# Kernel optimization log

Hardware: AMD Instinct MI355X
Metric: run time of the kernel (lower is better)

The kernel has to match this reference:

```python
import jax, jax.numpy as jnp
import numpy as np

B, SIZE, TRACK = 4096, 1024, 1024  # batch, input size, tracker_size


def setup_inputs() -> dict:
    key = jax.random.key(0)
    ks = jax.random.split(key, 9)
    s = 0.02  # small init scale to keep gates in a sane range
    return {
        "top_buf_h": jax.random.normal(ks[0], (B, SIZE), jnp.float32),
        "top_stack1_h": jax.random.normal(ks[1], (B, SIZE), jnp.float32),
        "top_stack2_h": jax.random.normal(ks[2], (B, SIZE), jnp.float32),
        "h_prev": jax.random.normal(ks[3], (B, TRACK), jnp.float32),
        "c_prev": jax.random.normal(ks[4], (B, TRACK), jnp.float32),
        "W_buf": jax.random.normal(ks[5], (SIZE, 4 * TRACK), jnp.float32) * s,
        "W_stack1": jax.random.normal(ks[6], (SIZE, 4 * TRACK), jnp.float32) * s,
        "W_stack2": jax.random.normal(ks[7], (SIZE, 4 * TRACK), jnp.float32) * s,
        "W_lateral": jax.random.normal(ks[8], (TRACK, 4 * TRACK), jnp.float32) * s,
        "b_lateral": jnp.zeros((4 * TRACK,), jnp.float32),
    }


def reference(top_buf_h, top_stack1_h, top_stack2_h, h_prev, c_prev,
              W_buf, W_stack1, W_stack2, W_lateral, b_lateral):
    # Fused tracker step: 3 bias-free projections + lateral projection (with bias)
    gates = (top_buf_h @ W_buf
             + top_stack1_h @ W_stack1
             + top_stack2_h @ W_stack2
             + h_prev @ W_lateral
             + b_lateral)                      # [B, 4*TRACK]
    # SPINN lstm(c_prev, gates): chunk order (a, i, f, o)
    a, i, f, o = jnp.split(gates, 4, axis=1)
    c = jnp.tanh(a) * jax.nn.sigmoid(i) + jax.nn.sigmoid(f) * c_prev
    h = jax.nn.sigmoid(o) * jnp.tanh(c)
    return (h, c)
```

## Files before the change

### kernel.cpp

```cpp
#include <hip/hip_runtime.h>


typedef __bf16 bf16x8 __attribute__((ext_vector_type(8)));
typedef float  f32x4  __attribute__((ext_vector_type(4)));

__device__ __forceinline__ unsigned short f2bf(float x) {
    unsigned int u = __builtin_bit_cast(unsigned int, x);
    u = (u + 0x7fffu + ((u >> 16) & 1u)) >> 16;
    return (unsigned short)u;
}

__device__ __forceinline__ void gl2lds16(const unsigned short* g, unsigned short* l) {
    __builtin_amdgcn_global_load_lds(
        (const __attribute__((address_space(1))) unsigned int*)g,
        (__attribute__((address_space(3))) unsigned int*)l,
        16, 0, 0);
}

__device__ __forceinline__ float sigf(float x) {
    return __builtin_amdgcn_rcpf(1.f + __expf(-x));
}
__device__ __forceinline__ float tanh_fast(float x) {
    return 2.f * __builtin_amdgcn_rcpf(1.f + __expf(-2.f * x)) - 1.f;
}


__global__ void convert_AB(const float* __restrict__ A0, const float* __restrict__ A1,
                           const float* __restrict__ A2, const float* __restrict__ A3,
                           const float* __restrict__ Wb, const float* __restrict__ W1,
                           const float* __restrict__ W2, const float* __restrict__ Wl,
                           unsigned short* __restrict__ Abf,
                           unsigned short* __restrict__ Bt) {
    __shared__ float t[32][33];
    if (blockIdx.x < 16384) {
        int idx = blockIdx.x * 256 + threadIdx.x;
        int e0  = idx * 4;
        int b   = e0 >> 12;
        int k   = e0 & 4095;
        const float* S = (k < 1024) ? A0 : (k < 2048) ? A1 : (k < 3072) ? A2 : A3;
        int col = k & 1023;
        const float4 v = *reinterpret_cast<const float4*>(S + (size_t)b * 1024 + col);
        ushort4 o;
        o.x = f2bf(v.x); o.y = f2bf(v.y); o.z = f2bf(v.z); o.w = f2bf(v.w);
        *reinterpret_cast<ushort4*>(Abf + (size_t)b * 4096 + k) = o;
    } else {
        int tile = blockIdx.x - 16384;
        int jt = tile & 127, kt = tile >> 7;
        int j0 = jt * 32, k0 = kt * 32;
        int ksel = k0 >> 10;
        const float* S = (ksel == 0) ? Wb : (ksel == 1) ? W1 : (ksel == 2) ? W2 : Wl;
        int kloc = k0 & 1023;
        int tx = threadIdx.x & 31, ty = threadIdx.x >> 5;
#pragma unroll
        for (int i = 0; i < 4; ++i) {
            int r = ty + i * 8;
            t[r][tx] = S[(size_t)(kloc + r) * 4096 + j0 + tx];
        }
        __syncthreads();
        int g = j0 >> 10;
        int nbase = j0 & 1023;
#pragma unroll
        for (int i = 0; i < 4; ++i) {
            int jj = ty + i * 8;
            int u  = nbase + jj;
            int p  = (u >> 6) * 256 + ((u >> 4) & 3) * 64 + g * 16 + (u & 15);
            Bt[(size_t)p * 4096 + k0 + tx] = f2bf(t[tx][jj]);
        }
    }
}


__global__ __launch_bounds__(512, 2) void gemm_lstm(
        const unsigned short* __restrict__ A,
        const unsigned short* __restrict__ Bt,
        const float* __restrict__ bias,
        const float* __restrict__ cprev,
        float* __restrict__ out) {
    __shared__ unsigned short lds[65536];
#define ASB(b) (lds + (b) * 16384)
#define BSB(b) (lds + 32768 + (b) * 16384)

    const int tid  = threadIdx.x;
    const int wid  = tid >> 6;
    const int lane = tid & 63;
    const int wm = wid >> 2, wn = wid & 3;
    const int lr = lane & 15, lq = lane >> 4;
    const int bm = blockIdx.y, bc = blockIdx.x;

    const int X0 = wid * 1024 + lane * 16;
    const int rs = X0 >> 7;
    const int cs = ((X0 & 127) ^ ((rs & 7) << 4)) >> 1;
    const unsigned short* Agb = A  + ((size_t)(bm * 256 + rs)) * 4096 + cs;
    const unsigned short* Bgb = Bt + ((size_t)(bc * 256 + rs)) * 4096 + cs;

    const int swz = (lr & 7) << 4;
    const int ca0 = ((lq * 16) ^ swz) >> 1;
    const int ca1 = ((64 + lq * 16) ^ swz) >> 1;

    f32x4 acc[8][4] = {};

#define STAGE_A(b, h, kt) do {                                               \
        unsigned short* _d = ASB(b) + (h) * 8192 + wid * 512;                \
        const unsigned short* _s = Agb + (size_t)((h) * 128) * 4096 + (kt) * 64; \
        gl2lds16(_s, _d);                                                    \
        gl2lds16(_s + 64 * 4096, _d + 4096);                                 \
    } while (0)
#define STAGE_B(b, h, kt) do {                                               \
        unsigned short* _d = BSB(b) + (h) * 8192 + wid * 512;                \
        const unsigned short* _s = Bgb + (size_t)((h) * 128) * 4096 + (kt) * 64; \
        gl2lds16(_s, _d);                                                    \
        gl2lds16(_s + 64 * 4096, _d + 4096);                                 \
    } while (0)
#define LDA(buf, mi, cax) (*reinterpret_cast<const bf16x8*>((buf) + (wm * 128 + (mi) * 16 + lr) * 64 + (cax)))
#define LDB(buf, ni, cax) (*reinterpret_cast<const bf16x8*>((buf) + (wn * 64  + (ni) * 16 + lr) * 64 + (cax)))
#define RD_A(DST, BUF, MI0) do {                                             \
        _Pragma("unroll")                                                    \
        for (int m = 0; m < 2; ++m) {                                        \
            DST[m][0] = LDA(BUF, (MI0) + m, ca0);                            \
            DST[m][1] = LDA(BUF, (MI0) + m, ca1);                            \
        } } while (0)
#define RD_B(DST, BUF) do {                                                  \
        _Pragma("unroll")                                                    \
        for (int n = 0; n < 4; ++n) {                                        \
            DST[n][0] = LDB(BUF, n, ca0);                                    \
            DST[n][1] = LDB(BUF, n, ca1);                                    \
        } } while (0)
#define SBAR() __builtin_amdgcn_s_barrier()
#define VMFENCE() asm volatile("s_waitcnt vmcnt(4)" ::: "memory")
#define MFMA16(P, AF, BF)                                                    \
        __builtin_amdgcn_s_setprio(1);                                       \
        _Pragma("unroll")                                                    \
        for (int m = 0; m < 2; ++m)                                          \
        _Pragma("unroll")                                                    \
        for (int ks = 0; ks < 2; ++ks)                                       \
        _Pragma("unroll")                                                    \
        for (int ni = 0; ni < 4; ++ni)                                       \
            acc[(P)*2 + m][ni] = __builtin_amdgcn_mfma_f32_16x16x32_bf16(    \
                AF[m][ks], BF[ni][ks], acc[(P)*2 + m][ni], 0, 0, 0);         \
        __builtin_amdgcn_s_setprio(0)

#define KITER(T, PAR) do {                                                   \
        const unsigned short* Ac = ASB(PAR);                                 \
        const unsigned short* Bc = BSB(PAR);                                 \
        const int ktA = ((T) < 63) ? (T) + 1 : 63;                           \
        const int ktB = ((T) < 62) ? (T) + 2 : 63;                           \
        STAGE_A(PAR ^ 1, 0, ktA);                                            \
        STAGE_A(PAR ^ 1, 1, ktA);                                            \
        bf16x8 bfr[4][2];                                                    \
        bf16x8 af[2][2];                                                     \
        RD_B(bfr, Bc);                                                       \
        RD_A(af, Ac, 0);                                                     \
        MFMA16(0, af, bfr);                                                  \
        SBAR();     \
        STAGE_B(PAR, 0, ktB);                                                \
        STAGE_B(PAR, 1, ktB);                                                \
        RD_A(af, Ac, 2);                                                     \
        MFMA16(1, af, bfr);                                                  \
        RD_A(af, Ac, 4);                                                     \
        MFMA16(2, af, bfr);                                                  \
        RD_A(af, Ac, 6);                                                     \
        MFMA16(3, af, bfr);                                                  \
        VMFENCE();                                                           \
        SBAR();                          \
    } while (0)

    STAGE_A(0, 0, 0); STAGE_A(0, 1, 0);
    STAGE_B(0, 0, 0); STAGE_B(0, 1, 0);
    STAGE_B(1, 0, 1); STAGE_B(1, 1, 1);
    VMFENCE();
    SBAR();

    for (int u = 0; u < 32; ++u) {
        KITER(2 * u, 0);
        KITER(2 * u + 1, 1);
    }

    const int un = bc * 64 + wn * 16 + lr;
    const float ba  = bias[un];
    const float bi  = bias[1024 + un];
    const float bfv = bias[2048 + un];
    const float bo  = bias[3072 + un];
    float* outh = out;
    float* outc = out + (size_t)4096 * 1024;

#pragma unroll
    for (int mi = 0; mi < 8; ++mi) {
        const int r0 = bm * 256 + wm * 128 + mi * 16 + lq * 4;
#pragma unroll
        for (int r = 0; r < 4; ++r) {
            const size_t off = (size_t)(r0 + r) * 1024 + un;
            const float a  = acc[mi][0][r] + ba;
            const float ii = acc[mi][1][r] + bi;
            const float ff = acc[mi][2][r] + bfv;
            const float oo = acc[mi][3][r] + bo;
            const float c  = tanh_fast(a) * sigf(ii) + sigf(ff) * cprev[off];
            outh[off] = sigf(oo) * tanh_fast(c);
            outc[off] = c;
        }
    }
#undef STAGE_A
#undef STAGE_B
#undef LDA
#undef LDB
#undef RD_A
#undef RD_B
#undef SBAR
#undef VMFENCE
#undef MFMA16
#undef KITER
#undef ASB
#undef BSB
}


extern "C" void kernel_launch(void* const* d_in, const int* in_sizes, int n_in,
                              void* d_out, int out_size, void* d_ws, size_t ws_size,
                              hipStream_t stream) {
    const float* top_buf = (const float*)d_in[0];
    const float* s1      = (const float*)d_in[1];
    const float* s2      = (const float*)d_in[2];
    const float* hprev   = (const float*)d_in[3];
    const float* cprev   = (const float*)d_in[4];
    const float* Wb      = (const float*)d_in[5];
    const float* W1      = (const float*)d_in[6];
    const float* W2      = (const float*)d_in[7];
    const float* Wl      = (const float*)d_in[8];
    const float* bl      = (const float*)d_in[9];

    unsigned short* Abf = (unsigned short*)d_ws;
    unsigned short* Bt  = Abf + (size_t)4096 * 4096;

    convert_AB<<<32768, 256, 0, stream>>>(top_buf, s1, s2, hprev,
                                          Wb, W1, W2, Wl, Abf, Bt);

    dim3 grid(16, 16);
    gemm_lstm<<<grid, 512, 0, stream>>>(Abf, Bt, bl, cprev, (float*)d_out);
}
```

Measured before the change: 147.7 us.

## Switch GEMM to 32x32x16 MFMA with 4x2 warp tiling and repacked weights

Replaces the 16x16x32 bf16 MFMA tiles with 32x32x16 MFMAs. The warp grid changes from 2x4 to 4x2 (64 rows by 128 columns per wave), and the weight repack permutation changes so each 32-column group keeps the four gates aligned. The K loop now does four k-steps per stage with a full LDS wait before the barrier, instead of interleaving the B-stage issue mid-compute. The aim is more work per MFMA issue and fewer LDS fragment reads per FLOP. The cost is less overlap between the staging loads and the math.

Result: slower. 164.1 us (+11.1%).

```diff
diff --git a/kernel.cpp b/kernel.cpp
--- a/kernel.cpp
+++ b/kernel.cpp
@@ -2,7 +2,7 @@
 
 
 typedef __bf16 bf16x8 __attribute__((ext_vector_type(8)));
-typedef float  f32x4  __attribute__((ext_vector_type(4)));
+typedef float  f32x16 __attribute__((ext_vector_type(16)));
 
 __device__ __forceinline__ unsigned short f2bf(float x) {
     unsigned int u = __builtin_bit_cast(unsigned int, x);
@@ -63,7 +63,7 @@
         for (int i = 0; i < 4; ++i) {
             int jj = ty + i * 8;
             int u  = nbase + jj;
-            int p  = (u >> 6) * 256 + ((u >> 4) & 3) * 64 + g * 16 + (u & 15);
+            int p  = (u >> 5) * 128 + g * 32 + (u & 31);
             Bt[(size_t)p * 4096 + k0 + tx] = f2bf(t[tx][jj]);
         }
     }
@@ -83,8 +83,8 @@
     const int tid  = threadIdx.x;
     const int wid  = tid >> 6;
     const int lane = tid & 63;
-    const int wm = wid >> 2, wn = wid & 3;
-    const int lr = lane & 15, lq = lane >> 4;
+    const int wm = wid >> 1, wn = wid & 1;
+    const int l31 = lane & 31, q5 = lane >> 5;
     const int bm = blockIdx.y, bc = blockIdx.x;
 
     const int X0 = wid * 1024 + lane * 16;
@@ -93,11 +93,12 @@
     const unsigned short* Agb = A  + ((size_t)(bm * 256 + rs)) * 4096 + cs;
     const unsigned short* Bgb = Bt + ((size_t)(bc * 256 + rs)) * 4096 + cs;
 
-    const int swz = (lr & 7) << 4;
-    const int ca0 = ((lq * 16) ^ swz) >> 1;
-    const int ca1 = ((64 + lq * 16) ^ swz) >> 1;
-
-    f32x4 acc[8][4] = {};
+    int ca32[4];
+#pragma unroll
+    for (int ks = 0; ks < 4; ++ks)
+        ca32[ks] = ((q5 * 16 + ks * 32) ^ ((lane & 7) << 4)) >> 1;
+
+    f32x16 acc[2][4] = {};
 
 #define STAGE_A(b, h, kt) do {                                               \
         unsigned short* _d = ASB(b) + (h) * 8192 + wid * 512;                \
@@ -111,33 +112,10 @@
         gl2lds16(_s, _d);                                                    \
         gl2lds16(_s + 64 * 4096, _d + 4096);                                 \
     } while (0)
-#define LDA(buf, mi, cax) (*reinterpret_cast<const bf16x8*>((buf) + (wm * 128 + (mi) * 16 + lr) * 64 + (cax)))
-#define LDB(buf, ni, cax) (*reinterpret_cast<const bf16x8*>((buf) + (wn * 64  + (ni) * 16 + lr) * 64 + (cax)))
-#define RD_A(DST, BUF, MI0) do {                                             \
-        _Pragma("unroll")                                                    \
-        for (int m = 0; m < 2; ++m) {                                        \
-            DST[m][0] = LDA(BUF, (MI0) + m, ca0);                            \
-            DST[m][1] = LDA(BUF, (MI0) + m, ca1);                            \
-        } } while (0)
-#define RD_B(DST, BUF) do {                                                  \
-        _Pragma("unroll")                                                    \
-        for (int n = 0; n < 4; ++n) {                                        \
-            DST[n][0] = LDB(BUF, n, ca0);                                    \
-            DST[n][1] = LDB(BUF, n, ca1);                                    \
-        } } while (0)
+#define LDA32(buf, mi, cax) (*reinterpret_cast<const bf16x8*>((buf) + (wm * 64 + (mi) * 32 + l31) * 64 + (cax)))
+#define LDB32(buf, ni, cax) (*reinterpret_cast<const bf16x8*>((buf) + (wn * 128 + (ni) * 32 + l31) * 64 + (cax)))
 #define SBAR() __builtin_amdgcn_s_barrier()
 #define VMFENCE() asm volatile("s_waitcnt vmcnt(4)" ::: "memory")
-#define MFMA16(P, AF, BF)                                                    \
-        __builtin_amdgcn_s_setprio(1);                                       \
-        _Pragma("unroll")                                                    \
-        for (int m = 0; m < 2; ++m)                                          \
-        _Pragma("unroll")                                                    \
-        for (int ks = 0; ks < 2; ++ks)                                       \
-        _Pragma("unroll")                                                    \
-        for (int ni = 0; ni < 4; ++ni)                                       \
-            acc[(P)*2 + m][ni] = __builtin_amdgcn_mfma_f32_16x16x32_bf16(    \
-                AF[m][ks], BF[ni][ks], acc[(P)*2 + m][ni], 0, 0, 0);         \
-        __builtin_amdgcn_s_setprio(0)
 
 #define KITER(T, PAR) do {                                                   \
         const unsigned short* Ac = ASB(PAR);                                 \
@@ -146,20 +124,28 @@
         const int ktB = ((T) < 62) ? (T) + 2 : 63;                           \
         STAGE_A(PAR ^ 1, 0, ktA);                                            \
         STAGE_A(PAR ^ 1, 1, ktA);                                            \
-        bf16x8 bfr[4][2];                                                    \
-        bf16x8 af[2][2];                                                     \
-        RD_B(bfr, Bc);                                                       \
-        RD_A(af, Ac, 0);                                                     \
-        MFMA16(0, af, bfr);                                                  \
-        SBAR();     \
+        _Pragma("unroll")                                                    \
+        for (int ks = 0; ks < 4; ++ks) {                                     \
+            bf16x8 bfr[4];                                                   \
+            bf16x8 af[2];                                                    \
+            _Pragma("unroll")                                                \
+            for (int ni = 0; ni < 4; ++ni) bfr[ni] = LDB32(Bc, ni, ca32[ks]);\
+            _Pragma("unroll")                                                \
+            for (int m = 0; m < 2; ++m)   af[m] = LDA32(Ac, m, ca32[ks]);    \
+            __builtin_amdgcn_s_setprio(1);                                   \
+            _Pragma("unroll")                                                \
+            for (int m = 0; m < 2; ++m)                                      \
+            _Pragma("unroll")                                                \
+            for (int ni = 0; ni < 4; ++ni)                                   \
+                acc[m][ni] = __builtin_amdgcn_mfma_f32_32x32x16_bf16(        \
+                    af[m], bfr[ni], acc[m][ni], 0, 0, 0);                    \
+            __builtin_amdgcn_s_setprio(0);                                   \
+        }                                                                    \
+        asm volatile("s_waitcnt lgkmcnt(0)");                                \
+        __builtin_amdgcn_sched_barrier(0);                                   \
+        SBAR();    \
         STAGE_B(PAR, 0, ktB);                                                \
         STAGE_B(PAR, 1, ktB);                                                \
-        RD_A(af, Ac, 2);                                                     \
-        MFMA16(1, af, bfr);                                                  \
-        RD_A(af, Ac, 4);                                                     \
-        MFMA16(2, af, bfr);                                                  \
-        RD_A(af, Ac, 6);                                                     \
-        MFMA16(3, af, bfr);                                                  \
         VMFENCE();                                                           \
         SBAR();                          \
     } while (0)
@@ -175,7 +161,7 @@
         KITER(2 * u + 1, 1);
     }
 
-    const int un = bc * 64 + wn * 16 + lr;
+    const int un = bc * 64 + wn * 32 + l31;
     const float ba  = bias[un];
     const float bi  = bias[1024 + un];
     const float bfv = bias[2048 + un];
@@ -184,15 +170,16 @@
     float* outc = out + (size_t)4096 * 1024;
 
 #pragma unroll
-    for (int mi = 0; mi < 8; ++mi) {
-        const int r0 = bm * 256 + wm * 128 + mi * 16 + lq * 4;
-#pragma unroll
-        for (int r = 0; r < 4; ++r) {
-            const size_t off = (size_t)(r0 + r) * 1024 + un;
-            const float a  = acc[mi][0][r] + ba;
-            const float ii = acc[mi][1][r] + bi;
-            const float ff = acc[mi][2][r] + bfv;
-            const float oo = acc[mi][3][r] + bo;
+    for (int mi = 0; mi < 2; ++mi) {
+        const int r0 = bm * 256 + wm * 64 + mi * 32 + 4 * q5;
+#pragma unroll
+        for (int reg = 0; reg < 16; ++reg) {
+            const int row = r0 + (reg & 3) + 8 * (reg >> 2);
+            const size_t off = (size_t)row * 1024 + un;
+            const float a  = acc[mi][0][reg] + ba;
+            const float ii = acc[mi][1][reg] + bi;
+            const float ff = acc[mi][2][reg] + bfv;
+            const float oo = acc[mi][3][reg] + bo;
             const float c  = tanh_fast(a) * sigf(ii) + sigf(ff) * cprev[off];
             outh[off] = sigf(oo) * tanh_fast(c);
             outc[off] = c;
@@ -200,13 +187,10 @@
     }
 #undef STAGE_A
 #undef STAGE_B
-#undef LDA
-#undef LDB
-#undef RD_A
-#undef RD_B
+#undef LDA32
+#undef LDB32
 #undef SBAR
 #undef VMFENCE
-#undef MFMA16
 #undef KITER
 #undef ASB
 #undef BSB
```

## Load B fragments directly from global memory into registers, bypassing LDS

Applied to the files above, without the earlier changes.

Removes the LDS double-buffer for the B (weight) tile: each wave now reads its bf16x8 B fragments straight from global memory at the start of every K iteration. The mid-iteration barrier and B staging disappear, and LDS use halves, which could allow a second resident block per CU. In exchange, B loads are no longer prefetched ahead of use. Waves sharing the same column slice each fetch it from global separately, and every iteration now waits for all outstanding loads (vmcnt(0)), so global latency may be exposed.

Result: slower. 226.1 us (+53.1%).

```diff
diff --git a/kernel.cpp b/kernel.cpp
--- a/kernel.cpp
+++ b/kernel.cpp
@@ -76,9 +76,8 @@
         const float* __restrict__ bias,
         const float* __restrict__ cprev,
         float* __restrict__ out) {
-    __shared__ unsigned short lds[65536];
+    __shared__ unsigned short lds[32768];
 #define ASB(b) (lds + (b) * 16384)
-#define BSB(b) (lds + 32768 + (b) * 16384)
 
     const int tid  = threadIdx.x;
     const int wid  = tid >> 6;
@@ -90,8 +89,9 @@
     const int X0 = wid * 1024 + lane * 16;
     const int rs = X0 >> 7;
     const int cs = ((X0 & 127) ^ ((rs & 7) << 4)) >> 1;
-    const unsigned short* Agb = A  + ((size_t)(bm * 256 + rs)) * 4096 + cs;
-    const unsigned short* Bgb = Bt + ((size_t)(bc * 256 + rs)) * 4096 + cs;
+    const unsigned short* Agb = A + ((size_t)(bm * 256 + rs)) * 4096 + cs;
+
+    const unsigned short* Bg = Bt + ((size_t)(bc * 256 + wn * 64 + lr)) * 4096 + lq * 8;
 
     const int swz = (lr & 7) << 4;
     const int ca0 = ((lq * 16) ^ swz) >> 1;
@@ -105,28 +105,14 @@
         gl2lds16(_s, _d);                                                    \
         gl2lds16(_s + 64 * 4096, _d + 4096);                                 \
     } while (0)
-#define STAGE_B(b, h, kt) do {                                               \
-        unsigned short* _d = BSB(b) + (h) * 8192 + wid * 512;                \
-        const unsigned short* _s = Bgb + (size_t)((h) * 128) * 4096 + (kt) * 64; \
-        gl2lds16(_s, _d);                                                    \
-        gl2lds16(_s + 64 * 4096, _d + 4096);                                 \
-    } while (0)
 #define LDA(buf, mi, cax) (*reinterpret_cast<const bf16x8*>((buf) + (wm * 128 + (mi) * 16 + lr) * 64 + (cax)))
-#define LDB(buf, ni, cax) (*reinterpret_cast<const bf16x8*>((buf) + (wn * 64  + (ni) * 16 + lr) * 64 + (cax)))
 #define RD_A(DST, BUF, MI0) do {                                             \
         _Pragma("unroll")                                                    \
         for (int m = 0; m < 2; ++m) {                                        \
             DST[m][0] = LDA(BUF, (MI0) + m, ca0);                            \
             DST[m][1] = LDA(BUF, (MI0) + m, ca1);                            \
         } } while (0)
-#define RD_B(DST, BUF) do {                                                  \
-        _Pragma("unroll")                                                    \
-        for (int n = 0; n < 4; ++n) {                                        \
-            DST[n][0] = LDB(BUF, n, ca0);                                    \
-            DST[n][1] = LDB(BUF, n, ca1);                                    \
-        } } while (0)
 #define SBAR() __builtin_amdgcn_s_barrier()
-#define VMFENCE() asm volatile("s_waitcnt vmcnt(4)" ::: "memory")
 #define MFMA16(P, AF, BF)                                                    \
         __builtin_amdgcn_s_setprio(1);                                       \
         _Pragma("unroll")                                                    \
@@ -141,33 +127,31 @@
 
 #define KITER(T, PAR) do {                                                   \
         const unsigned short* Ac = ASB(PAR);                                 \
-        const unsigned short* Bc = BSB(PAR);                                 \
         const int ktA = ((T) < 63) ? (T) + 1 : 63;                           \
-        const int ktB = ((T) < 62) ? (T) + 2 : 63;                           \
-        STAGE_A(PAR ^ 1, 0, ktA);                                            \
+        STAGE_A(PAR ^ 1, 0, ktA);                  \
         STAGE_A(PAR ^ 1, 1, ktA);                                            \
         bf16x8 bfr[4][2];                                                    \
+        _Pragma("unroll")                                                    \
+        for (int ni = 0; ni < 4; ++ni)                                       \
+        _Pragma("unroll")                                                    \
+        for (int ks = 0; ks < 2; ++ks)                                       \
+            bfr[ni][ks] = *reinterpret_cast<const bf16x8*>(                  \
+                Bg + (size_t)ni * 65536 + (T) * 64 + ks * 32);               \
         bf16x8 af[2][2];                                                     \
-        RD_B(bfr, Bc);                                                       \
         RD_A(af, Ac, 0);                                                     \
         MFMA16(0, af, bfr);                                                  \
-        SBAR();     \
-        STAGE_B(PAR, 0, ktB);                                                \
-        STAGE_B(PAR, 1, ktB);                                                \
         RD_A(af, Ac, 2);                                                     \
         MFMA16(1, af, bfr);                                                  \
         RD_A(af, Ac, 4);                                                     \
         MFMA16(2, af, bfr);                                                  \
         RD_A(af, Ac, 6);                                                     \
         MFMA16(3, af, bfr);                                                  \
-        VMFENCE();                                                           \
-        SBAR();                          \
+        asm volatile("s_waitcnt vmcnt(0)" ::: "memory");   \
+        SBAR();                                                              \
     } while (0)
 
     STAGE_A(0, 0, 0); STAGE_A(0, 1, 0);
-    STAGE_B(0, 0, 0); STAGE_B(0, 1, 0);
-    STAGE_B(1, 0, 1); STAGE_B(1, 1, 1);
-    VMFENCE();
+    asm volatile("s_waitcnt vmcnt(0)" ::: "memory");
     SBAR();
 
     for (int u = 0; u < 32; ++u) {
@@ -199,17 +183,12 @@
         }
     }
 #undef STAGE_A
-#undef STAGE_B
 #undef LDA
-#undef LDB
 #undef RD_A
-#undef RD_B
 #undef SBAR
-#undef VMFENCE
 #undef MFMA16
 #undef KITER
 #undef ASB
-#undef BSB
 }
 
 
```

## Split K-iteration into four barrier-synchronized phases interleaving LDS reads, staging and MFMA

Applied to the files above, without the earlier changes.

Restructures each K iteration into four phases. Each phase issues LDS fragment reads plus one global-to-LDS stage, waits on lgkmcnt, crosses a workgroup barrier, then runs a block of MFMAs. Sched_barrier fences pin the instruction order so the compiler cannot merge or reorder the phases. The aim is to spread the global loads across the iteration and keep waves in lockstep so memory and matrix work overlap. The cost is many extra s_barriers per iteration, which can stall waves and reduce latency hiding.

Measured after the change: 151.5 us. 2.6% more time.

```diff
diff --git a/kernel.cpp b/kernel.cpp
--- a/kernel.cpp
+++ b/kernel.cpp
@@ -125,7 +125,10 @@
             DST[n][0] = LDB(BUF, n, ca0);                                    \
             DST[n][1] = LDB(BUF, n, ca1);                                    \
         } } while (0)
-#define SBAR() __builtin_amdgcn_s_barrier()
+#define SBAR()   __builtin_amdgcn_s_barrier()
+#define SPIN()   __builtin_amdgcn_sched_barrier(0)
+#define LGK0()   asm volatile("s_waitcnt lgkmcnt(0)")
+#define LGK8()   asm volatile("s_waitcnt lgkmcnt(8)")
 #define VMFENCE() asm volatile("s_waitcnt vmcnt(4)" ::: "memory")
 #define MFMA16(P, AF, BF)                                                    \
         __builtin_amdgcn_s_setprio(1);                                       \
@@ -144,24 +147,51 @@
         const unsigned short* Bc = BSB(PAR);                                 \
         const int ktA = ((T) < 63) ? (T) + 1 : 63;                           \
         const int ktB = ((T) < 62) ? (T) + 2 : 63;                           \
-        STAGE_A(PAR ^ 1, 0, ktA);                                            \
-        STAGE_A(PAR ^ 1, 1, ktA);                                            \
         bf16x8 bfr[4][2];                                                    \
         bf16x8 af[2][2];                                                     \
+                             \
         RD_B(bfr, Bc);                                                       \
         RD_A(af, Ac, 0);                                                     \
+        STAGE_A(PAR ^ 1, 0, ktA);                                            \
+        LGK8();                                                              \
+        SPIN();                                                              \
+        SBAR();                                                              \
+        LGK0();                                                              \
+        SPIN();                                                              \
         MFMA16(0, af, bfr);                                                  \
-        SBAR();     \
+        SPIN();                                                              \
+        SBAR();                                                              \
+                              \
+        RD_A(af, Ac, 2);                                                     \
+        STAGE_A(PAR ^ 1, 1, ktA);                                            \
+        SPIN();                                                              \
+        SBAR();                                                              \
+        LGK0();                                                              \
+        SPIN();                                                              \
+        MFMA16(1, af, bfr);                                                  \
+        SPIN();                                                              \
+        SBAR();                                                              \
+        \
+        RD_A(af, Ac, 4);                                                     \
         STAGE_B(PAR, 0, ktB);                                                \
+        SPIN();                                                              \
+        SBAR();                                                              \
+        LGK0();                                                              \
+        SPIN();                                                              \
+        MFMA16(2, af, bfr);                                                  \
+        SPIN();                                                              \
+        SBAR();                                                              \
+         \
+        RD_A(af, Ac, 6);                                                     \
         STAGE_B(PAR, 1, ktB);                                                \
-        RD_A(af, Ac, 2);                                                     \
-        MFMA16(1, af, bfr);                                                  \
-        RD_A(af, Ac, 4);                                                     \
-        MFMA16(2, af, bfr);                                                  \
-        RD_A(af, Ac, 6);                                                     \
+        SPIN();                                                              \
+        SBAR();                                                              \
+        LGK0();                                                              \
+        SPIN();                                                              \
         MFMA16(3, af, bfr);                                                  \
-        VMFENCE();                                                           \
-        SBAR();                          \
+        SPIN();                                                              \
+        VMFENCE();           \
+        SBAR();                                                              \
     } while (0)
 
     STAGE_A(0, 0, 0); STAGE_A(0, 1, 0);
@@ -205,6 +235,9 @@
 #undef RD_A
 #undef RD_B
 #undef SBAR
+#undef SPIN
+#undef LGK0
+#undef LGK8
 #undef VMFENCE
 #undef MFMA16
 #undef KITER
```
